# Kernel tuning notes

Hardware: AMD Instinct MI355X
Metric: run time of the kernel (lower is better)

Reference implementation:

```python
import jax, jax.numpy as jnp
import numpy as np

EMBED_DIM = 1024
NUM_HEADS = 16
HEAD_DIM = EMBED_DIM // NUM_HEADS
BATCH = 4
SEQ = 2048


def setup_inputs() -> dict:
    key = jax.random.key(0)
    k1, k2, k3 = jax.random.split(key, 3)
    scale = 0.02
    x = jax.random.normal(k1, (BATCH, SEQ, EMBED_DIM), dtype=jnp.float32)
    Wqkv = jax.random.normal(k2, (EMBED_DIM, 3 * EMBED_DIM), dtype=jnp.float32) * scale
    bqkv = jnp.zeros((3 * EMBED_DIM,), dtype=jnp.float32)
    Wout = jax.random.normal(k3, (EMBED_DIM, EMBED_DIM), dtype=jnp.float32) * scale
    bout = jnp.zeros((EMBED_DIM,), dtype=jnp.float32)
    # causal mask: 1 where attention is allowed (lower triangle), 0 elsewhere
    mask = jnp.tril(jnp.ones((SEQ, SEQ), dtype=jnp.int32))
    return {"x": x, "mask": mask, "Wqkv": Wqkv, "bqkv": bqkv, "Wout": Wout, "bout": bout}


def reference(x, mask, Wqkv, bqkv, Wout, bout):
    B, S, E = x.shape
    H, D = NUM_HEADS, HEAD_DIM
    qkv = x @ Wqkv + bqkv                      # [B,S,3E]
    qkv = qkv.reshape(B, S, 3, H, D)
    qkv = jnp.transpose(qkv, (2, 0, 3, 1, 4))  # [3,B,H,S,D]
    Q, K, V = qkv[0], qkv[1], qkv[2]
    scores = jnp.einsum('bhqd,bhkd->bhqk', Q, K) / jnp.sqrt(jnp.float32(D))
    scores = jnp.where(mask[None, None] == 0, jnp.float32(-jnp.inf), scores)
    attn = jax.nn.softmax(scores, axis=-1)     # dropout omitted (eval mode)
    out = jnp.einsum('bhqk,bhkd->bhqd', attn, V)
    out = jnp.transpose(out, (0, 2, 1, 3)).reshape(B, S, E)
    return out @ Wout + bout
```

## Files before the change

### kernel.cpp

```cpp
#include <hip/hip_runtime.h>

#define S_LEN 2048
#define NH    16
#define HD    64
#define EMB   1024
#define NB    4
#define MROWS (NB * S_LEN)

typedef __attribute__((ext_vector_type(8))) short  short8;
typedef __attribute__((ext_vector_type(4))) float  float4_t;
typedef __attribute__((ext_vector_type(4))) int    int4_t;
union U8 { int4_t i; short8 s; };

__device__ __forceinline__ unsigned short f2bf(float f) {
    unsigned int x = __float_as_uint(f);
    unsigned int r = (x + 0x7fffu + ((x >> 16) & 1u)) >> 16;
    return (unsigned short)r;
}

typedef const __attribute__((address_space(1))) unsigned int* gas_ptr;
typedef __attribute__((address_space(3))) unsigned int*       las_ptr;
__device__ __forceinline__ void gld_lds16(const void* g, void* l) {
    __builtin_amdgcn_global_load_lds((gas_ptr)g, (las_ptr)l, 16, 0, 0);
}

__global__ void cvt_f32_bf16(const float* __restrict__ in,
                             unsigned short* __restrict__ out, int n2) {
    int i = blockIdx.x * blockDim.x + threadIdx.x;
    if (i < n2) {
        float2 v = ((const float2*)in)[i];
        ushort2 o; o.x = f2bf(v.x); o.y = f2bf(v.y);
        ((ushort2*)out)[i] = o;
    }
}

__global__ void transpose_f32_bf16(const float* __restrict__ in,
                                   unsigned short* __restrict__ out, int R, int C) {
    __shared__ float tile[32][33];
    int n0 = blockIdx.x * 32, r0 = blockIdx.y * 32;
    int tx = threadIdx.x, ty = threadIdx.y;
#pragma unroll
    for (int i = 0; i < 4; ++i)
        tile[ty + i * 8][tx] = in[(size_t)(r0 + ty + i * 8) * C + n0 + tx];
    __syncthreads();
#pragma unroll
    for (int i = 0; i < 4; ++i)
        out[(size_t)(n0 + ty + i * 8) * R + r0 + tx] = f2bf(tile[tx][ty + i * 8]);
}

__global__ __launch_bounds__(256) void gemm_qkv(
    const unsigned short* __restrict__ X,
    const unsigned short* __restrict__ WT,
    const float* __restrict__ bias,
    unsigned short* __restrict__ Qb,
    unsigned short* __restrict__ Kb,
    unsigned short* __restrict__ VTb)
{
    __shared__ alignas(16) unsigned short As[128 * 32];
    __shared__ alignas(16) unsigned short Bs[128 * 32];
    const int K = 1024;
    int t = threadIdx.x;
    int wave = t >> 6, lane = t & 63, quad = lane >> 4, l = lane & 15;
    int bm = blockIdx.x * 128, bn = blockIdx.y * 128;
    int wm = (wave >> 1) * 64, wn = (wave & 1) * 64;

    float4_t z = {0.f, 0.f, 0.f, 0.f};
    float4_t acc[4][4];
#pragma unroll
    for (int i = 0; i < 4; ++i)
#pragma unroll
        for (int j = 0; j < 4; ++j) acc[i][j] = z;

    for (int kt = 0; kt < K / 32; ++kt) {
        int k0 = kt * 32;
        if (kt) __syncthreads();
#pragma unroll
        for (int it = 0; it < 2; ++it) {
            int c = t + 256 * it;
            int row = c >> 2, col = (c & 3) * 8;
            gld_lds16(&X [(size_t)(bm + row) * K + k0 + col], &As[c * 8]);
            gld_lds16(&WT[(size_t)(bn + row) * K + k0 + col], &Bs[c * 8]);
        }
        __syncthreads();
        short8 af[4], bfr[4];
#pragma unroll
        for (int i = 0; i < 4; ++i)
            af[i] = *(const short8*)&As[(wm + i * 16 + l) * 32 + quad * 8];
#pragma unroll
        for (int j = 0; j < 4; ++j)
            bfr[j] = *(const short8*)&Bs[(wn + j * 16 + l) * 32 + quad * 8];
#pragma unroll
        for (int i = 0; i < 4; ++i)
#pragma unroll
            for (int j = 0; j < 4; ++j)
                acc[i][j] = __builtin_amdgcn_mfma_f32_16x16x32_bf16(
                    af[i], bfr[j], acc[i][j], 0, 0, 0);
    }
#pragma unroll
    for (int j = 0; j < 4; ++j) {
        int gc = bn + wn + j * 16 + l;
        float bv = bias[gc];
        int which = gc >> 10, rem = gc & 1023;
        int h = rem >> 6, d = rem & 63;
        if (which == 2) {
            int bb = bm >> 11;
            size_t rowbase = ((size_t)(bb * NH + h) * HD + d) * S_LEN;
#pragma unroll
            for (int i = 0; i < 4; ++i) {
                unsigned int u0 = __float_as_uint(acc[i][j][0] + bv) + 0x8000u;
                unsigned int u1 = __float_as_uint(acc[i][j][1] + bv) + 0x8000u;
                unsigned int u2 = __float_as_uint(acc[i][j][2] + bv) + 0x8000u;
                unsigned int u3 = __float_as_uint(acc[i][j][3] + bv) + 0x8000u;
                uint2 vv;
                vv.x = __builtin_amdgcn_perm(u1, u0, 0x07060302u);
                vv.y = __builtin_amdgcn_perm(u3, u2, 0x07060302u);
                int s0 = (bm + wm + i * 16 + quad * 4) & 2047;
                *(uint2*)&VTb[rowbase + s0] = vv;
            }
        } else {
#pragma unroll
            for (int i = 0; i < 4; ++i)
#pragma unroll
                for (int r = 0; r < 4; ++r) {
                    int gr = bm + wm + i * 16 + quad * 4 + r;
                    int b = gr >> 11, s = gr & 2047;
                    unsigned short ov = f2bf(acc[i][j][r] + bv);
                    size_t bh2 = (size_t)(b * NH + h);
                    if (which == 0) Qb[(bh2 * S_LEN + s) * HD + d] = ov;
                    else            Kb[(bh2 * S_LEN + s) * HD + d] = ov;
                }
        }
    }
}

__global__ __launch_bounds__(256) void flash_attn(
    const unsigned short* __restrict__ Qb,
    const unsigned short* __restrict__ Kb,
    const unsigned short* __restrict__ VTb,
    unsigned short* __restrict__ AO)
{
    __shared__ alignas(16) unsigned short smem[8192];
    unsigned short* Kbuf = smem;
    unsigned short* Vbuf = smem + 4096;

    int t = threadIdx.x, wave = t >> 6, lane = t & 63, quad = lane >> 4, cl = lane & 15;
    int blk = blockIdx.x;
    int bh = (blk & 7) + 8 * ((blk >> 3) & 7);
    int g4 = blk >> 6;
    int ci = g4 * 4 + wave;
    int b = bh >> 4, h = bh & 15;
    int qb = 32 * ci;
    int nkt = ((qb + 31) >> 6) + 1;
    int nkt_max = ((32 * (g4 * 4 + 3) + 31) >> 6) + 1;

    const unsigned short* Qbase = Qb  + (size_t)bh * S_LEN * HD;
    const unsigned short* Kbase = Kb  + (size_t)bh * S_LEN * HD;
    const unsigned short* Vbase = VTb + (size_t)bh * HD * S_LEN;

    float4_t z = {0.f, 0.f, 0.f, 0.f};
    short8 bQ[2][2];
#pragma unroll
    for (int qt = 0; qt < 2; ++qt)
#pragma unroll
        for (int hh = 0; hh < 2; ++hh)
            bQ[qt][hh] = *(const short8*)&Qbase[(size_t)(qb + qt * 16 + cl) * HD + hh * 32 + quad * 8];

    float4_t acc[2][4];
#pragma unroll
    for (int qt = 0; qt < 2; ++qt)
#pragma unroll
        for (int nb = 0; nb < 4; ++nb) acc[qt][nb] = z;
    float ps[2] = {0.f, 0.f};

    const char* Kc = (const char*)Kbuf;
    const char* Vc = (const char*)Vbuf;
    int koff0[4], koff1[4];
#pragma unroll
    for (int t4 = 0; t4 < 4; ++t4) {
        int row = t4 * 16 + cl, sw = row & 7;
        koff0[t4] = (row << 7) | ((quad ^ sw) << 4);
        koff1[t4] = (row << 7) | (((quad + 4) ^ sw) << 4);
    }
    int voff[2][4][2];
#pragma unroll
    for (int p = 0; p < 2; ++p)
#pragma unroll
        for (int nb = 0; nb < 4; ++nb) {
            int row = nb * 16 + cl, sw = row & 7;
            int bo = p * 64 + quad * 8, bo2 = bo + 32;
            voff[p][nb][0] = (row << 7) | (((bo >> 4) ^ sw) << 4) | (bo & 15);
            voff[p][nb][1] = (row << 7) | (((bo2 >> 4) ^ sw) << 4) | (bo2 & 15);
        }

    for (int kt = 0; kt < nkt_max; ++kt) {
        int key0 = kt << 6;
        if (kt) __syncthreads();
#pragma unroll
        for (int i = 0; i < 2; ++i) {
            int s = t + 256 * i;
            int row = s >> 3, c16 = (s & 7) ^ (row & 7);
            gld_lds16(&Kbase[(size_t)(key0 + row) * HD + c16 * 8], &Kbuf[s * 8]);
            gld_lds16(&Vbase[(size_t)row * S_LEN + key0 + c16 * 8], &Vbuf[s * 8]);
        }
        __syncthreads();

        if (kt < nkt) {
            short8 aK0[4], aK1[4];
#pragma unroll
            for (int t4 = 0; t4 < 4; ++t4) {
                aK0[t4] = *(const short8*)(Kc + koff0[t4]);
                aK1[t4] = *(const short8*)(Kc + koff1[t4]);
            }
            uint2 bvlo[2][4], bvhi[2][4];
#pragma unroll
            for (int p = 0; p < 2; ++p)
#pragma unroll
                for (int nb = 0; nb < 4; ++nb) {
                    bvlo[p][nb] = *(const uint2*)(Vc + voff[p][nb][0]);
                    bvhi[p][nb] = *(const uint2*)(Vc + voff[p][nb][1]);
                }

            bool diag = (kt == nkt - 1);
#pragma unroll
            for (int qt = 0; qt < 2; ++qt) {
                unsigned int pk[4][2];
#pragma unroll
                for (int t4 = 0; t4 < 4; ++t4) {
                    float4_t st = __builtin_amdgcn_mfma_f32_16x16x32_bf16(
                        aK1[t4], bQ[qt][1],
                        __builtin_amdgcn_mfma_f32_16x16x32_bf16(aK0[t4], bQ[qt][0], z, 0, 0, 0),
                        0, 0, 0);
                    unsigned int u[4];
#pragma unroll
                    for (int r = 0; r < 4; ++r) {
                        float e = __expf(st[r] * 0.125f);
                        if (diag) {
                            int key = key0 + t4 * 16 + quad * 4 + r;
                            e = (key <= qb + qt * 16 + cl) ? e : 0.f;
                        }
                        ps[qt] += e;
                        u[r] = __float_as_uint(e) + 0x8000u;
                    }
                    pk[t4][0] = __builtin_amdgcn_perm(u[1], u[0], 0x07060302u);
                    pk[t4][1] = __builtin_amdgcn_perm(u[3], u[2], 0x07060302u);
                }
#pragma unroll
                for (int p = 0; p < 2; ++p) {
                    U8 a; a.i = (int4_t){(int)pk[2 * p][0], (int)pk[2 * p][1],
                                         (int)pk[2 * p + 1][0], (int)pk[2 * p + 1][1]};
#pragma unroll
                    for (int nb = 0; nb < 4; ++nb) {
                        U8 bb; bb.i = (int4_t){(int)bvlo[p][nb].x, (int)bvlo[p][nb].y,
                                               (int)bvhi[p][nb].x, (int)bvhi[p][nb].y};
                        acc[qt][nb] = __builtin_amdgcn_mfma_f32_16x16x32_bf16(
                            a.s, bb.s, acc[qt][nb], 0, 0, 0);
                    }
                }
            }
        }
    }

    __syncthreads();
    unsigned short* stgw = smem + wave * (16 * 68);

#pragma unroll
    for (int qt = 0; qt < 2; ++qt) {
        float s = ps[qt];
        s += __shfl_xor(s, 16);
        s += __shfl_xor(s, 32);
        float inv = 1.f / s;
        float fr[4];
#pragma unroll
        for (int r = 0; r < 4; ++r) fr[r] = __shfl(inv, quad * 4 + r);
#pragma unroll
        for (int nb = 0; nb < 4; ++nb)
#pragma unroll
            for (int r = 0; r < 4; ++r) {
                unsigned int u = __float_as_uint(acc[qt][nb][r] * fr[r]) + 0x8000u;
                stgw[(quad * 4 + r) * 68 + nb * 16 + cl] = (unsigned short)(u >> 16);
            }
#pragma unroll
        for (int pass = 0; pass < 4; ++pass) {
            int idx = pass * 64 + lane;
            int row = idx >> 4, part = idx & 15;
            ushort4 v = *(const ushort4*)&stgw[row * 68 + part * 4];
            *(ushort4*)&AO[((size_t)b * S_LEN + qb + qt * 16 + row) * EMB + h * HD + part * 4] = v;
        }
    }
}

__global__ __launch_bounds__(256) void gemm_out(
    const unsigned short* __restrict__ A,
    const unsigned short* __restrict__ WT,
    const float* __restrict__ bias,
    float* __restrict__ out)
{
    __shared__ alignas(16) unsigned short As[128 * 32];
    __shared__ alignas(16) unsigned short Bs[128 * 32];
    const int K = 1024;
    int t = threadIdx.x;
    int wave = t >> 6, lane = t & 63, quad = lane >> 4, l = lane & 15;
    int bm = blockIdx.x * 128, bn = blockIdx.y * 128;
    int wm = (wave >> 1) * 64, wn = (wave & 1) * 64;

    float4_t z = {0.f, 0.f, 0.f, 0.f};
    float4_t acc[4][4];
#pragma unroll
    for (int i = 0; i < 4; ++i)
#pragma unroll
        for (int j = 0; j < 4; ++j) acc[i][j] = z;

    for (int kt = 0; kt < K / 32; ++kt) {
        int k0 = kt * 32;
        if (kt) __syncthreads();
#pragma unroll
        for (int it = 0; it < 2; ++it) {
            int c = t + 256 * it;
            int row = c >> 2, col = (c & 3) * 8;
            gld_lds16(&A [(size_t)(bm + row) * K + k0 + col], &As[c * 8]);
            gld_lds16(&WT[(size_t)(bn + row) * K + k0 + col], &Bs[c * 8]);
        }
        __syncthreads();
        short8 af[4], bfr[4];
#pragma unroll
        for (int i = 0; i < 4; ++i)
            af[i] = *(const short8*)&As[(wm + i * 16 + l) * 32 + quad * 8];
#pragma unroll
        for (int j = 0; j < 4; ++j)
            bfr[j] = *(const short8*)&Bs[(wn + j * 16 + l) * 32 + quad * 8];
#pragma unroll
        for (int i = 0; i < 4; ++i)
#pragma unroll
            for (int j = 0; j < 4; ++j)
                acc[i][j] = __builtin_amdgcn_mfma_f32_16x16x32_bf16(
                    af[i], bfr[j], acc[i][j], 0, 0, 0);
    }
#pragma unroll
    for (int j = 0; j < 4; ++j) {
        int gc = bn + wn + j * 16 + l;
        float bv = bias[gc];
#pragma unroll
        for (int i = 0; i < 4; ++i) {
#pragma unroll
            for (int r = 0; r < 4; ++r) {
                int gr = bm + wm + i * 16 + quad * 4 + r;
                out[(size_t)gr * EMB + gc] = acc[i][j][r] + bv;
            }
        }
    }
}

extern "C" void kernel_launch(void* const* d_in, const int* in_sizes, int n_in,
                              void* d_out, int out_size, void* d_ws, size_t ws_size,
                              hipStream_t stream) {
    const float* x    = (const float*)d_in[0];
    const float* Wqkv = (const float*)d_in[2];
    const float* bqkv = (const float*)d_in[3];
    const float* Wout = (const float*)d_in[4];
    const float* bout = (const float*)d_in[5];
    float* out = (float*)d_out;

    char* ws = (char*)d_ws;
    const size_t SZ = (size_t)NB * NH * S_LEN * HD * 2;
    unsigned short* Qb    = (unsigned short*)(ws);
    unsigned short* Kb    = (unsigned short*)(ws + SZ);
    unsigned short* VTb   = (unsigned short*)(ws + 2 * SZ);
    unsigned short* Xb    = (unsigned short*)(ws + 3 * SZ);
    unsigned short* AO    = (unsigned short*)(ws + 3 * SZ);
    unsigned short* WqkvT = (unsigned short*)(ws + 4 * SZ);
    unsigned short* WoutT = (unsigned short*)(ws + 4 * SZ + (size_t)3 * EMB * EMB * 2);

    int n2 = MROWS * EMB / 2;
    cvt_f32_bf16<<<dim3((n2 + 255) / 256), 256, 0, stream>>>(x, Xb, n2);
    dim3 tb(32, 8);
    transpose_f32_bf16<<<dim3(3 * EMB / 32, EMB / 32), tb, 0, stream>>>(Wqkv, WqkvT, EMB, 3 * EMB);
    transpose_f32_bf16<<<dim3(EMB / 32, EMB / 32), tb, 0, stream>>>(Wout, WoutT, EMB, EMB);
    gemm_qkv<<<dim3(MROWS / 128, 3 * EMB / 128), 256, 0, stream>>>(Xb, WqkvT, bqkv, Qb, Kb, VTb);
    flash_attn<<<dim3(1024), 256, 0, stream>>>(Qb, Kb, VTb, AO);
    gemm_out<<<dim3(MROWS / 128, EMB / 128), 256, 0, stream>>>(AO, WoutT, bout, out);
}
```

Before: 289.3 us.

## Pair causal query chunks per block with double-buffered K/V staging

New measurement: 315.7 us. 1.09x slower.

```diff
diff --git a/kernel.cpp b/kernel.cpp
--- a/kernel.cpp
+++ b/kernel.cpp
@@ -23,6 +23,8 @@
 __device__ __forceinline__ void gld_lds16(const void* g, void* l) {
     __builtin_amdgcn_global_load_lds((gas_ptr)g, (las_ptr)l, 16, 0, 0);
 }
+
+#define QSCALE 0.18033688011112042f
 
 __global__ void cvt_f32_bf16(const float* __restrict__ in,
                              unsigned short* __restrict__ out, int n2) {
@@ -124,10 +126,10 @@
                 for (int r = 0; r < 4; ++r) {
                     int gr = bm + wm + i * 16 + quad * 4 + r;
                     int b = gr >> 11, s = gr & 2047;
-                    unsigned short ov = f2bf(acc[i][j][r] + bv);
+                    float ov = acc[i][j][r] + bv;
                     size_t bh2 = (size_t)(b * NH + h);
-                    if (which == 0) Qb[(bh2 * S_LEN + s) * HD + d] = ov;
-                    else            Kb[(bh2 * S_LEN + s) * HD + d] = ov;
+                    if (which == 0) Qb[(bh2 * S_LEN + s) * HD + d] = f2bf(ov * QSCALE);
+                    else            Kb[(bh2 * S_LEN + s) * HD + d] = f2bf(ov);
                 }
         }
     }
@@ -139,41 +141,31 @@
     const unsigned short* __restrict__ VTb,
     unsigned short* __restrict__ AO)
 {
-    __shared__ alignas(16) unsigned short smem[8192];
-    unsigned short* Kbuf = smem;
-    unsigned short* Vbuf = smem + 4096;
+    __shared__ alignas(16) unsigned short smem[16384 + 4 * 16 * 68];
 
     int t = threadIdx.x, wave = t >> 6, lane = t & 63, quad = lane >> 4, cl = lane & 15;
     int blk = blockIdx.x;
     int bh = (blk & 7) + 8 * ((blk >> 3) & 7);
-    int g4 = blk >> 6;
-    int ci = g4 * 4 + wave;
+    int j = blk >> 6;
     int b = bh >> 4, h = bh & 15;
-    int qb = 32 * ci;
-    int nkt = ((qb + 31) >> 6) + 1;
-    int nkt_max = ((32 * (g4 * 4 + 3) + 31) >> 6) + 1;
+    int ci1 = 4 * j + wave;
+    int ci2 = 63 - ci1;
+    int n1 = (ci1 >> 1) + 1;
+    int n2 = (ci2 >> 1) + 1;
+    int n1max = 2 * j + 2;
+    int n2max = 32 - 2 * j;
+    int T = n1max + n2max;
 
     const unsigned short* Qbase = Qb  + (size_t)bh * S_LEN * HD;
     const unsigned short* Kbase = Kb  + (size_t)bh * S_LEN * HD;
     const unsigned short* Vbase = VTb + (size_t)bh * HD * S_LEN;
+    unsigned short* stgw = smem + 16384 + wave * (16 * 68);
 
     float4_t z = {0.f, 0.f, 0.f, 0.f};
-    short8 bQ[2][2];
-#pragma unroll
-    for (int qt = 0; qt < 2; ++qt)
-#pragma unroll
-        for (int hh = 0; hh < 2; ++hh)
-            bQ[qt][hh] = *(const short8*)&Qbase[(size_t)(qb + qt * 16 + cl) * HD + hh * 32 + quad * 8];
-
-    float4_t acc[2][4];
-#pragma unroll
-    for (int qt = 0; qt < 2; ++qt)
-#pragma unroll
-        for (int nb = 0; nb < 4; ++nb) acc[qt][nb] = z;
-    float ps[2] = {0.f, 0.f};
-
-    const char* Kc = (const char*)Kbuf;
-    const char* Vc = (const char*)Vbuf;
+    short8 onesf;
+#pragma unroll
+    for (int i = 0; i < 8; ++i) onesf[i] = (short)0x3F80;
+
     int koff0[4], koff1[4];
 #pragma unroll
     for (int t4 = 0; t4 < 4; ++t4) {
@@ -192,101 +184,138 @@
             voff[p][nb][1] = (row << 7) | (((bo2 >> 4) ^ sw) << 4) | (bo2 & 15);
         }
 
-    for (int kt = 0; kt < nkt_max; ++kt) {
+    auto stage = [&](int u) {
+        int kt = (u < n1max) ? u : (u - n1max);
         int key0 = kt << 6;
-        if (kt) __syncthreads();
+        unsigned short* Kd = smem + (u & 1) * 8192;
+        unsigned short* Vd = Kd + 4096;
 #pragma unroll
         for (int i = 0; i < 2; ++i) {
             int s = t + 256 * i;
             int row = s >> 3, c16 = (s & 7) ^ (row & 7);
-            gld_lds16(&Kbase[(size_t)(key0 + row) * HD + c16 * 8], &Kbuf[s * 8]);
-            gld_lds16(&Vbase[(size_t)row * S_LEN + key0 + c16 * 8], &Vbuf[s * 8]);
-        }
+            gld_lds16(&Kbase[(size_t)(key0 + row) * HD + c16 * 8], &Kd[s * 8]);
+            gld_lds16(&Vbase[(size_t)row * S_LEN + key0 + c16 * 8], &Vd[s * 8]);
+        }
+    };
+
+    short8 bQ[2][2];
+    auto loadQ = [&](int qbx) {
+#pragma unroll
+        for (int qt = 0; qt < 2; ++qt)
+#pragma unroll
+            for (int hh = 0; hh < 2; ++hh)
+                bQ[qt][hh] = *(const short8*)&Qbase[(size_t)(qbx + qt * 16 + cl) * HD + hh * 32 + quad * 8];
+    };
+
+    float4_t acc[2][4], accs[2];
+    auto reset = [&]() {
+#pragma unroll
+        for (int qt = 0; qt < 2; ++qt) {
+            accs[qt] = z;
+#pragma unroll
+            for (int nb = 0; nb < 4; ++nb) acc[qt][nb] = z;
+        }
+    };
+
+    auto compute = [&](int u, int kt, int qbx, bool diag) {
+        const char* Kc = (const char*)(smem + (u & 1) * 8192);
+        const char* Vc = Kc + 8192;
+        int key0 = kt << 6;
+        short8 aK0[4], aK1[4];
+#pragma unroll
+        for (int t4 = 0; t4 < 4; ++t4) {
+            aK0[t4] = *(const short8*)(Kc + koff0[t4]);
+            aK1[t4] = *(const short8*)(Kc + koff1[t4]);
+        }
+        uint2 bvlo[2][4], bvhi[2][4];
+#pragma unroll
+        for (int p = 0; p < 2; ++p)
+#pragma unroll
+            for (int nb = 0; nb < 4; ++nb) {
+                bvlo[p][nb] = *(const uint2*)(Vc + voff[p][nb][0]);
+                bvhi[p][nb] = *(const uint2*)(Vc + voff[p][nb][1]);
+            }
+#pragma unroll
+        for (int qt = 0; qt < 2; ++qt) {
+            unsigned int pk[4][2];
+#pragma unroll
+            for (int t4 = 0; t4 < 4; ++t4) {
+                float4_t st = __builtin_amdgcn_mfma_f32_16x16x32_bf16(
+                    aK1[t4], bQ[qt][1],
+                    __builtin_amdgcn_mfma_f32_16x16x32_bf16(aK0[t4], bQ[qt][0], z, 0, 0, 0),
+                    0, 0, 0);
+                unsigned int u4[4];
+#pragma unroll
+                for (int r = 0; r < 4; ++r) {
+                    float e = __builtin_amdgcn_exp2f(st[r]);
+                    if (diag) {
+                        int key = key0 + t4 * 16 + quad * 4 + r;
+                        e = (key <= qbx + qt * 16 + cl) ? e : 0.f;
+                    }
+                    u4[r] = __float_as_uint(e) + 0x8000u;
+                }
+                pk[t4][0] = __builtin_amdgcn_perm(u4[1], u4[0], 0x07060302u);
+                pk[t4][1] = __builtin_amdgcn_perm(u4[3], u4[2], 0x07060302u);
+            }
+#pragma unroll
+            for (int p = 0; p < 2; ++p) {
+                U8 a; a.i = (int4_t){(int)pk[2 * p][0], (int)pk[2 * p][1],
+                                     (int)pk[2 * p + 1][0], (int)pk[2 * p + 1][1]};
+                accs[qt] = __builtin_amdgcn_mfma_f32_16x16x32_bf16(
+                    a.s, onesf, accs[qt], 0, 0, 0);
+#pragma unroll
+                for (int nb = 0; nb < 4; ++nb) {
+                    U8 bb; bb.i = (int4_t){(int)bvlo[p][nb].x, (int)bvlo[p][nb].y,
+                                           (int)bvhi[p][nb].x, (int)bvhi[p][nb].y};
+                    acc[qt][nb] = __builtin_amdgcn_mfma_f32_16x16x32_bf16(
+                        a.s, bb.s, acc[qt][nb], 0, 0, 0);
+                }
+            }
+        }
+    };
+
+    auto flushf = [&](int qbx) {
+#pragma unroll
+        for (int qt = 0; qt < 2; ++qt) {
+            float fr[4];
+#pragma unroll
+            for (int r = 0; r < 4; ++r) fr[r] = 1.f / accs[qt][r];
+#pragma unroll
+            for (int nb = 0; nb < 4; ++nb)
+#pragma unroll
+                for (int r = 0; r < 4; ++r) {
+                    unsigned int uu = __float_as_uint(acc[qt][nb][r] * fr[r]) + 0x8000u;
+                    stgw[(quad * 4 + r) * 68 + nb * 16 + cl] = (unsigned short)(uu >> 16);
+                }
+#pragma unroll
+            for (int pass = 0; pass < 4; ++pass) {
+                int idx = pass * 64 + lane;
+                int row = idx >> 4, part = idx & 15;
+                ushort4 v = *(const ushort4*)&stgw[row * 68 + part * 4];
+                *(ushort4*)&AO[((size_t)b * S_LEN + qbx + qt * 16 + row) * EMB + h * HD + part * 4] = v;
+            }
+        }
+    };
+
+    loadQ(32 * ci1);
+    reset();
+    stage(0);
+    for (int u = 0; u < T; ++u) {
         __syncthreads();
-
-        if (kt < nkt) {
-            short8 aK0[4], aK1[4];
-#pragma unroll
-            for (int t4 = 0; t4 < 4; ++t4) {
-                aK0[t4] = *(const short8*)(Kc + koff0[t4]);
-                aK1[t4] = *(const short8*)(Kc + koff1[t4]);
-            }
-            uint2 bvlo[2][4], bvhi[2][4];
-#pragma unroll
-            for (int p = 0; p < 2; ++p)
-#pragma unroll
-                for (int nb = 0; nb < 4; ++nb) {
-                    bvlo[p][nb] = *(const uint2*)(Vc + voff[p][nb][0]);
-                    bvhi[p][nb] = *(const uint2*)(Vc + voff[p][nb][1]);
-                }
-
-            bool diag = (kt == nkt - 1);
-#pragma unroll
-            for (int qt = 0; qt < 2; ++qt) {
-                unsigned int pk[4][2];
-#pragma unroll
-                for (int t4 = 0; t4 < 4; ++t4) {
-                    float4_t st = __builtin_amdgcn_mfma_f32_16x16x32_bf16(
-                        aK1[t4], bQ[qt][1],
-                        __builtin_amdgcn_mfma_f32_16x16x32_bf16(aK0[t4], bQ[qt][0], z, 0, 0, 0),
-                        0, 0, 0);
-                    unsigned int u[4];
-#pragma unroll
-                    for (int r = 0; r < 4; ++r) {
-                        float e = __expf(st[r] * 0.125f);
-                        if (diag) {
-                            int key = key0 + t4 * 16 + quad * 4 + r;
-                            e = (key <= qb + qt * 16 + cl) ? e : 0.f;
-                        }
-                        ps[qt] += e;
-                        u[r] = __float_as_uint(e) + 0x8000u;
-                    }
-                    pk[t4][0] = __builtin_amdgcn_perm(u[1], u[0], 0x07060302u);
-                    pk[t4][1] = __builtin_amdgcn_perm(u[3], u[2], 0x07060302u);
-                }
-#pragma unroll
-                for (int p = 0; p < 2; ++p) {
-                    U8 a; a.i = (int4_t){(int)pk[2 * p][0], (int)pk[2 * p][1],
-                                         (int)pk[2 * p + 1][0], (int)pk[2 * p + 1][1]};
-#pragma unroll
-                    for (int nb = 0; nb < 4; ++nb) {
-                        U8 bb; bb.i = (int4_t){(int)bvlo[p][nb].x, (int)bvlo[p][nb].y,
-                                               (int)bvhi[p][nb].x, (int)bvhi[p][nb].y};
-                        acc[qt][nb] = __builtin_amdgcn_mfma_f32_16x16x32_bf16(
-                            a.s, bb.s, acc[qt][nb], 0, 0, 0);
-                    }
-                }
-            }
-        }
-    }
-
-    __syncthreads();
-    unsigned short* stgw = smem + wave * (16 * 68);
-
-#pragma unroll
-    for (int qt = 0; qt < 2; ++qt) {
-        float s = ps[qt];
-        s += __shfl_xor(s, 16);
-        s += __shfl_xor(s, 32);
-        float inv = 1.f / s;
-        float fr[4];
-#pragma unroll
-        for (int r = 0; r < 4; ++r) fr[r] = __shfl(inv, quad * 4 + r);
-#pragma unroll
-        for (int nb = 0; nb < 4; ++nb)
-#pragma unroll
-            for (int r = 0; r < 4; ++r) {
-                unsigned int u = __float_as_uint(acc[qt][nb][r] * fr[r]) + 0x8000u;
-                stgw[(quad * 4 + r) * 68 + nb * 16 + cl] = (unsigned short)(u >> 16);
-            }
-#pragma unroll
-        for (int pass = 0; pass < 4; ++pass) {
-            int idx = pass * 64 + lane;
-            int row = idx >> 4, part = idx & 15;
-            ushort4 v = *(const ushort4*)&stgw[row * 68 + part * 4];
-            *(ushort4*)&AO[((size_t)b * S_LEN + qb + qt * 16 + row) * EMB + h * HD + part * 4] = v;
-        }
-    }
+        if (u + 1 < T) stage(u + 1);
+        if (u < n1max) {
+            if (u < n1) compute(u, u, 32 * ci1, u == n1 - 1);
+        } else {
+            if (u == n1max) {
+                flushf(32 * ci1);
+                loadQ(32 * ci2);
+                reset();
+            }
+            int kt = u - n1max;
+            if (kt < n2) compute(u, kt, 32 * ci2, kt == n2 - 1);
+        }
+    }
+    flushf(32 * ci2);
 }
 
 __global__ __launch_bounds__(256) void gemm_out(
@@ -376,6 +405,6 @@
     transpose_f32_bf16<<<dim3(3 * EMB / 32, EMB / 32), tb, 0, stream>>>(Wqkv, WqkvT, EMB, 3 * EMB);
     transpose_f32_bf16<<<dim3(EMB / 32, EMB / 32), tb, 0, stream>>>(Wout, WoutT, EMB, EMB);
     gemm_qkv<<<dim3(MROWS / 128, 3 * EMB / 128), 256, 0, stream>>>(Xb, WqkvT, bqkv, Qb, Kb, VTb);
-    flash_attn<<<dim3(1024), 256, 0, stream>>>(Qb, Kb, VTb, AO);
+    flash_attn<<<dim3(512), 256, 0, stream>>>(Qb, Kb, VTb, AO);
     gemm_out<<<dim3(MROWS / 128, EMB / 128), 256, 0, stream>>>(AO, WoutT, bout, out);
 }
```
